# Kernel tuning notes

Measured on AMD Instinct MI355X. Metric: run time of the kernel, lower is better.

The kernel has to match this reference:

```python
import jax, jax.numpy as jnp
import numpy as np

B, N, E = 4, 2048, 1024
A, H = 64, 16          # attention_feature_dim, heads
D = A                   # per-head dim per source's rearrange quirk: d = attention_feature_dim
DK = A / H              # source scales by sqrt(attention_feature_dim / heads) = sqrt(4)
NEG_INF = jnp.float32(-jnp.inf)


def setup_inputs() -> dict:
    key = jax.random.key(0)
    ks = jax.random.split(key, 6)
    x = jax.random.normal(ks[0], (B, N, E), dtype=jnp.float32)
    mask = jax.random.randint(ks[1], (B, N), 0, 2, dtype=jnp.int32)
    # nn.Linear(E, A*H*3): weight [out,in] -> store transposed [in,out] for x @ W
    w_qkv = jax.random.normal(ks[2], (E, A * H * 3), dtype=jnp.float32) / np.sqrt(E)
    b_qkv = jax.random.normal(ks[3], (A * H * 3,), dtype=jnp.float32) * 0.02
    w_out = jax.random.normal(ks[4], (A * H, E), dtype=jnp.float32) / np.sqrt(A * H)
    b_out = jax.random.normal(ks[5], (E,), dtype=jnp.float32) * 0.02
    return {"x": x, "mask": mask, "w_qkv": w_qkv, "b_qkv": b_qkv,
            "w_out": w_out, "b_out": b_out}


def reference(x, mask, w_qkv, b_qkv, w_out, b_out):
    b, n, _ = x.shape
    qkv = x @ w_qkv + b_qkv                         # [b, n, 3*H*D]
    q, k, v = jnp.split(qkv, 3, axis=-1)            # each [b, n, H*D]
    def to_heads(t):
        return t.reshape(b, n, H, D).transpose(0, 2, 1, 3)  # [b, H, n, D]
    q, k, v = to_heads(q), to_heads(k), to_heads(v)
    scale = jnp.float32(1.0 / np.sqrt(DK))
    scores = jnp.einsum('bhqd,bhkd->bhqk', q, k) * scale    # [b, H, n, n]
    # mask: [b, n] -> [b, 1, 1, n]; masked positions (==0) get -inf
    scores = jnp.where(mask[:, None, None, :] == 0, NEG_INF, scores)
    attn = jax.nn.softmax(scores, axis=-1)
    out = jnp.einsum('bhqk,bhkd->bhqd', attn, v)            # [b, H, n, D]
    out = out.transpose(0, 2, 1, 3).reshape(b, n, H * D)    # [b, n, H*D]
    return out @ w_out + b_out                              # [b, n, E]
```

## Files before the change

### kernel.cpp

```cpp
#include <hip/hip_runtime.h>


typedef __bf16 bf16;
typedef __attribute__((ext_vector_type(8))) __bf16 bf16x8;
typedef __attribute__((ext_vector_type(4))) float f32x4;

#define MFMA16(a, b, c) __builtin_amdgcn_mfma_f32_16x16x32_bf16(a, b, c, 0, 0, 0)
#define GLOAD_LDS(src, dst) __builtin_amdgcn_global_load_lds( \
    (const __attribute__((address_space(1))) void*)(src),     \
    (__attribute__((address_space(3))) void*)(dst), 16, 0, 0)
#define BAR() __builtin_amdgcn_s_barrier()
#define VMCNT(n) asm volatile("s_waitcnt vmcnt(" #n ")" ::: "memory")

#define QSCALE 0.72134752f

__device__ __forceinline__ void transpose_tile(
    const float* __restrict__ in, bf16* __restrict__ out, int R, int C,
    int scale_rows, float scale, int bx, int by, int t, float (*s)[65])
{
    const int r0 = by * 64;
    const int c0 = bx * 64;
    const int tr  = t >> 4;
    const int tc4 = (t & 15) * 4;
#pragma unroll
    for (int p = 0; p < 4; ++p) {
        int r = tr + p * 16;
        float4 v = *(const float4*)(in + (size_t)(r0 + r) * C + c0 + tc4);
        s[r][tc4 + 0] = v.x; s[r][tc4 + 1] = v.y;
        s[r][tc4 + 2] = v.z; s[r][tc4 + 3] = v.w;
    }
    __syncthreads();
    const int cw  = t >> 3;
    const int rw8 = (t & 7) * 8;
#pragma unroll
    for (int p = 0; p < 2; ++p) {
        int c = cw + p * 32;
        float f = (c0 + c) < scale_rows ? scale : 1.0f;
        union { uint4 v; bf16 h[8]; } u;
#pragma unroll
        for (int j = 0; j < 8; ++j) u.h[j] = (bf16)(s[rw8 + j][c] * f);
        *(uint4*)(out + (size_t)(c0 + c) * R + r0 + rw8) = u.v;
    }
}

__global__ __launch_bounds__(256, 1) void prep_kernel(
    const float* __restrict__ x, bf16* __restrict__ xb,
    const float* __restrict__ w_qkv, bf16* __restrict__ wqkvT,
    const float* __restrict__ w_out, bf16* __restrict__ woutT)
{
    __shared__ float s[64][65];
    const int t = threadIdx.x;
    int blk = blockIdx.x;
    if (blk < 8192) {
        int i = blk * 256 + t;
        float4 v = *(const float4*)(x + (size_t)i * 4);
        union { ushort4 u; bf16 h[4]; } o;
        o.h[0] = (bf16)v.x; o.h[1] = (bf16)v.y;
        o.h[2] = (bf16)v.z; o.h[3] = (bf16)v.w;
        *(ushort4*)(xb + (size_t)i * 4) = o.u;
        return;
    }
    blk -= 8192;
    if (blk < 768) {
        transpose_tile(w_qkv, wqkvT, 1024, 3072, 1024, QSCALE,
                       blk % 48, blk / 48, t, s);
    } else {
        blk -= 768;
        transpose_tile(w_out, woutT, 1024, 1024, 0, 1.0f,
                       blk % 16, blk / 16, t, s);
    }
}

template <typename OutT>
__global__ __launch_bounds__(512, 2) void gemm128x256_kernel(
    const bf16* __restrict__ A, const bf16* __restrict__ Bt,
    const float* __restrict__ bias, OutT* __restrict__ C,
    int M, int N, int K, int qcols, float qscale, int nbx)
{
    __shared__ __align__(16) bf16 As[3 * 128 * 64];
    __shared__ __align__(16) bf16 Bs[3 * 256 * 64];

    const int t    = threadIdx.x;
    const int lane = t & 63;
    const int wave = t >> 6;
    const int wr   = wave >> 2;
    const int wc   = wave & 3;
    const int l15  = lane & 15;
    const int g    = lane >> 4;

    const int nwg  = gridDim.x;
    const int per  = nwg >> 3;
    const int mper = per / nbx;
    const int wg   = blockIdx.x;
    const int xcd  = wg & 7;
    const int idx  = wg >> 3;
    const int m0   = (xcd * mper + idx % mper) * 128;
    const int n0   = (idx / mper) * 256;

    const int ntile = K >> 6;

    int srow[2], sblk[2];
#pragma unroll
    for (int r = 0; r < 2; ++r) {
        int s = t * 16 + r * 8192;
        srow[r] = s >> 7;
        int blk = (s >> 4) & 7;
        sblk[r] = blk ^ (srow[r] & 7);
    }
    const int ldst0 = t * 8;

    const bf16* Abase = A  + (size_t)m0 * K;
    const bf16* Bbase = Bt + (size_t)n0 * K;

    const f32x4 z = {0.f, 0.f, 0.f, 0.f};
    f32x4 acc[4][4];
#pragma unroll
    for (int i = 0; i < 4; ++i)
#pragma unroll
        for (int j = 0; j < 4; ++j) acc[i][j] = z;

    auto stageA = [&](int tile, int slot) {
        if (tile >= ntile) return;
        bf16* dst = As + slot * 8192;
        const bf16* src = Abase + tile * 64;
#pragma unroll
        for (int r = 0; r < 2; ++r)
            GLOAD_LDS(src + (size_t)srow[r] * K + sblk[r] * 8,
                      dst + ldst0 + r * 4096);
    };
    auto stageBh = [&](int tile, int slot, int h) {
        if (tile >= ntile) return;
        bf16* dst = Bs + slot * 16384 + h * 8192;
        const bf16* src = Bbase + (size_t)(h * 128) * K + tile * 64;
#pragma unroll
        for (int r = 0; r < 2; ++r)
            GLOAD_LDS(src + (size_t)srow[r] * K + sblk[r] * 8,
                      dst + ldst0 + r * 4096);
    };

#define LOAD_AF(slot)                                                         \
    _Pragma("unroll")                                                         \
    for (int f = 0; f < 4; ++f) {                                             \
        int row = wr * 64 + f * 16 + l15;                                     \
        _Pragma("unroll")                                                     \
        for (int ks = 0; ks < 2; ++ks)                                        \
            af[f][ks] = *(const bf16x8*)(&As[(slot) * 8192 + row * 64 +       \
                            (((ks * 4 + g) ^ (row & 7)) * 8)]);               \
    }
#define LOAD_BF(slot, half, dstv)                                             \
    _Pragma("unroll")                                                         \
    for (int c2 = 0; c2 < 2; ++c2) {                                          \
        int row = wc * 64 + ((half) * 2 + c2) * 16 + l15;                     \
        _Pragma("unroll")                                                     \
        for (int ks = 0; ks < 2; ++ks)                                        \
            dstv[c2][ks] = *(const bf16x8*)(&Bs[(slot) * 16384 + row * 64 +   \
                            (((ks * 4 + g) ^ (row & 7)) * 8)]);               \
    }
#define MFMA_H(bv, half)                                                      \
    {                                                                         \
        __builtin_amdgcn_s_setprio(1);                                        \
        _Pragma("unroll")                                                     \
        for (int f = 0; f < 4; ++f)                                           \
            _Pragma("unroll")                                                 \
            for (int c2 = 0; c2 < 2; ++c2) {                                  \
                acc[f][(half) * 2 + c2] = MFMA16(                             \
                    af[f][0], bv[c2][0], acc[f][(half) * 2 + c2]);            \
                acc[f][(half) * 2 + c2] = MFMA16(                             \
                    af[f][1], bv[c2][1], acc[f][(half) * 2 + c2]);            \
            }                                                                 \
        __builtin_amdgcn_s_setprio(0);                                        \
    }

    stageA(0, 0); stageBh(0, 0, 0); stageBh(0, 0, 1);
    stageA(1, 1); stageBh(1, 1, 0); stageBh(1, 1, 1);
    VMCNT(6);
    BAR();

    int slot = 0;
    for (int T = 0; T < ntile; ++T) {
        int slot2 = slot + 2; if (slot2 >= 3) slot2 -= 3;
        bf16x8 af[4][2], blo[2][2], bhi[2][2];
        LOAD_AF(slot);
        LOAD_BF(slot, 0, blo);
        stageA(T + 2, slot2);
        stageBh(T + 2, slot2, 0);
        MFMA_H(blo, 0);
        BAR();
        LOAD_BF(slot, 1, bhi);
        stageBh(T + 2, slot2, 1);
        MFMA_H(bhi, 1);
        if (T + 1 < ntile) {
            if (T + 2 < ntile) { VMCNT(6); } else { VMCNT(0); }
        }
        BAR();
        slot = (slot == 2) ? 0 : slot + 1;
    }

#undef LOAD_AF
#undef LOAD_BF
#undef MFMA_H

#pragma unroll
    for (int f = 0; f < 4; ++f) {
        int row = m0 + wr * 64 + f * 16 + g * 4;
#pragma unroll
        for (int cf = 0; cf < 4; ++cf) {
            int col = n0 + wc * 64 + cf * 16 + l15;
            float bs = bias[col];
            if (col < qcols) bs *= qscale;
#pragma unroll
            for (int r = 0; r < 4; ++r) {
                float v = acc[f][cf][r] + bs;
                C[(size_t)(row + r) * N + col] = (OutT)v;
            }
        }
    }
}

__global__ __launch_bounds__(256, 1) void vtrans_kernel(
    const bf16* __restrict__ qkv, bf16* __restrict__ vtg)
{
    __shared__ float tile[64][65];
    const int t  = threadIdx.x;
    const int n0 = blockIdx.x * 64;
    const int bh = blockIdx.y;
    const int b  = bh >> 4, h = bh & 15;
    const bf16* src = qkv + (size_t)(b * 2048 + n0) * 3072 + 2048 + h * 64;
#pragma unroll
    for (int r = 0; r < 2; ++r) {
        int s = t + r * 256;
        int row = s >> 3, c8 = (s & 7) * 8;
        union { uint4 v; bf16 h8[8]; } u;
        u.v = *(const uint4*)(src + (size_t)row * 3072 + c8);
#pragma unroll
        for (int j = 0; j < 8; ++j) tile[row][c8 + j] = (float)u.h8[j];
    }
    __syncthreads();
    bf16* dst = vtg + (size_t)bh * (64 * 2048) + n0;
#pragma unroll
    for (int r = 0; r < 2; ++r) {
        int s = t + r * 256;
        int d = s >> 3, n8 = (s & 7) * 8;
        union { uint4 v; bf16 h8[8]; } o;
#pragma unroll
        for (int j = 0; j < 8; ++j) o.h8[j] = (bf16)tile[n8 + j][d];
        *(uint4*)(dst + (size_t)d * 2048 + n8) = o.v;
    }
}

__global__ __launch_bounds__(256, 3) void attn_kernel(
    const bf16* __restrict__ qkv, const bf16* __restrict__ vtg,
    const int* __restrict__ mask, bf16* __restrict__ O)
{
    __shared__ __align__(16) bf16 Ks[2][64 * 64];
    __shared__ __align__(16) bf16 Vt[2][64 * 64];
    __shared__ __align__(16) bf16 Ps[4][16 * 88];
    __shared__ __align__(16) float mneg[2048];

    const int t    = threadIdx.x;
    const int lane = t & 63;
    const int wave = t >> 6;
    const int l15  = lane & 15;
    const int g    = lane >> 4;

    const int bid = (blockIdx.x & 7) * 128 + (blockIdx.x >> 3);
    const int qt  = bid & 15;
    const int bh  = bid >> 4;
    const int h   = bh & 15;
    const int b   = bh >> 4;
    const int q0  = qt * 128 + wave * 16;

    const int* mrow = mask + b * 2048;
    for (int i = t; i < 2048; i += 256)
        mneg[i] = mrow[i] ? 0.0f : -1e30f;

    const size_t RS = 3072;
    const bf16* qp0 = qkv + (size_t)(b * 2048 + q0 + l15) * RS + h * 64 + g * 8;
    const bf16* qp1 = qp0 + (size_t)64 * RS;
    bf16x8 aQ[2][2];
    aQ[0][0] = *(const bf16x8*)(qp0);
    aQ[0][1] = *(const bf16x8*)(qp0 + 32);
    aQ[1][0] = *(const bf16x8*)(qp1);
    aQ[1][1] = *(const bf16x8*)(qp1 + 32);

    const bf16* kbase = qkv + (size_t)(b * 2048) * RS + 1024 + h * 64;
    const bf16* vbase = vtg + (size_t)bh * (64 * 2048);

    const int e0 = t * 8;
    int srow[2], scol[2];
#pragma unroll
    for (int r = 0; r < 2; ++r) {
        int e   = e0 + r * 2048;
        int row = e >> 6;
        int cb  = (e >> 3) & 7;
        srow[r] = row;
        scol[r] = ((cb ^ (row & 7)) * 8);
    }

    const int rb0 = ((g)     ^ (l15 & 7)) * 8;
    const int rb1 = ((4 + g) ^ (l15 & 7)) * 8;

    const f32x4 z = {0.f, 0.f, 0.f, 0.f};
    f32x4 o0[4] = {z, z, z, z}, o1[4] = {z, z, z, z};
    f32x4 lacc0 = z, lacc1 = z;

    bf16x8 ones;
#pragma unroll
    for (int j = 0; j < 8; ++j) ones[j] = (bf16)1.0f;

#pragma unroll
    for (int r = 0; r < 2; ++r) {
        GLOAD_LDS(kbase + (size_t)srow[r] * RS + scol[r],   &Ks[0][e0 + r * 2048]);
        GLOAD_LDS(vbase + (size_t)srow[r] * 2048 + scol[r], &Vt[0][e0 + r * 2048]);
    }
    asm volatile("s_waitcnt vmcnt(0)" ::: "memory");
    __syncthreads();

    for (int i = 0; i < 32; ++i) {
        const int kc  = i * 64;
        const int buf = i & 1;

        if (i + 1 < 32) {
#pragma unroll
            for (int r = 0; r < 2; ++r) {
                GLOAD_LDS(kbase + (size_t)(kc + 64 + srow[r]) * RS + scol[r],
                          &Ks[buf ^ 1][e0 + r * 2048]);
                GLOAD_LDS(vbase + (size_t)srow[r] * 2048 + kc + 64 + scol[r],
                          &Vt[buf ^ 1][e0 + r * 2048]);
            }
        }

        f32x4 mb4[4];
#pragma unroll
        for (int kt = 0; kt < 4; ++kt)
#pragma unroll
            for (int r = 0; r < 4; ++r)
                mb4[kt][r] = mneg[kc + kt * 16 + g * 4 + r];

        bf16x8 bk[4][2];
#pragma unroll
        for (int kt = 0; kt < 4; ++kt) {
            const bf16* kr = &Ks[buf][(kt * 16 + l15) * 64];
            bk[kt][0] = *(const bf16x8*)(kr + rb0);
            bk[kt][1] = *(const bf16x8*)(kr + rb1);
        }

        f32x4 S[4];
#pragma unroll
        for (int kt = 0; kt < 4; ++kt) {
            S[kt] = MFMA16(bk[kt][0], aQ[0][0], mb4[kt]);
            S[kt] = MFMA16(bk[kt][1], aQ[0][1], S[kt]);
        }
#pragma unroll
        for (int kt = 0; kt < 4; ++kt) {
            union { bf16 hh[4]; ushort4 u; } pk;
#pragma unroll
            for (int r = 0; r < 4; ++r)
                pk.hh[r] = (bf16)__builtin_amdgcn_exp2f(S[kt][r]);
            *(ushort4*)(&Ps[wave][l15 * 88 + kt * 16 + g * 4]) = pk.u;
        }
        asm volatile("s_waitcnt lgkmcnt(0)" ::: "memory");
        __builtin_amdgcn_sched_barrier(0);
        const bf16x8 aP00 = *(const bf16x8*)(&Ps[wave][l15 * 88 + g * 8]);
        const bf16x8 aP01 = *(const bf16x8*)(&Ps[wave][l15 * 88 + 32 + g * 8]);
        asm volatile("s_waitcnt lgkmcnt(0)" ::: "memory");
        __builtin_amdgcn_sched_barrier(0);

#pragma unroll
        for (int kt = 0; kt < 4; ++kt) {
            S[kt] = MFMA16(bk[kt][0], aQ[1][0], mb4[kt]);
            S[kt] = MFMA16(bk[kt][1], aQ[1][1], S[kt]);
        }

        bf16x8 bv[4][2];
#pragma unroll
        for (int dt = 0; dt < 4; ++dt) {
            const bf16* vr = &Vt[buf][(dt * 16 + l15) * 64];
            bv[dt][0] = *(const bf16x8*)(vr + rb0);
            bv[dt][1] = *(const bf16x8*)(vr + rb1);
        }

#pragma unroll
        for (int kt = 0; kt < 4; ++kt) {
            union { bf16 hh[4]; ushort4 u; } pk;
#pragma unroll
            for (int r = 0; r < 4; ++r)
                pk.hh[r] = (bf16)__builtin_amdgcn_exp2f(S[kt][r]);
            *(ushort4*)(&Ps[wave][l15 * 88 + kt * 16 + g * 4]) = pk.u;
        }

        lacc0 = MFMA16(aP00, ones, lacc0);
        lacc0 = MFMA16(aP01, ones, lacc0);
#pragma unroll
        for (int dt = 0; dt < 4; ++dt) {
            o0[dt] = MFMA16(aP00, bv[dt][0], o0[dt]);
            o0[dt] = MFMA16(aP01, bv[dt][1], o0[dt]);
        }
        asm volatile("s_waitcnt lgkmcnt(0)" ::: "memory");
        __builtin_amdgcn_sched_barrier(0);
        const bf16x8 aP10 = *(const bf16x8*)(&Ps[wave][l15 * 88 + g * 8]);
        const bf16x8 aP11 = *(const bf16x8*)(&Ps[wave][l15 * 88 + 32 + g * 8]);

        lacc1 = MFMA16(aP10, ones, lacc1);
        lacc1 = MFMA16(aP11, ones, lacc1);
#pragma unroll
        for (int dt = 0; dt < 4; ++dt) {
            o1[dt] = MFMA16(aP10, bv[dt][0], o1[dt]);
            o1[dt] = MFMA16(aP11, bv[dt][1], o1[dt]);
        }

        asm volatile("s_waitcnt vmcnt(0)" ::: "memory");
        __syncthreads();
    }

    float inv0[4], inv1[4];
#pragma unroll
    for (int r = 0; r < 4; ++r) {
        inv0[r] = 1.0f / fmaxf(lacc0[r], 1e-30f);
        inv1[r] = 1.0f / fmaxf(lacc1[r], 1e-30f);
    }
#pragma unroll
    for (int nt = 0; nt < 4; ++nt) {
#pragma unroll
        for (int r = 0; r < 4; ++r) {
            int d = nt * 16 + l15;
            int row0 = q0 + g * 4 + r;
            O[(size_t)(b * 2048 + row0) * 1024 + h * 64 + d] = (bf16)(o0[nt][r] * inv0[r]);
            O[(size_t)(b * 2048 + row0 + 64) * 1024 + h * 64 + d] = (bf16)(o1[nt][r] * inv1[r]);
        }
    }
}

extern "C" void kernel_launch(void* const* d_in, const int* in_sizes, int n_in,
                              void* d_out, int out_size, void* d_ws, size_t ws_size,
                              hipStream_t stream)
{
    const float* x     = (const float*)d_in[0];
    const int*   mask  = (const int*)d_in[1];
    const float* w_qkv = (const float*)d_in[2];
    const float* b_qkv = (const float*)d_in[3];
    const float* w_out = (const float*)d_in[4];
    const float* b_out = (const float*)d_in[5];
    float* out = (float*)d_out;

    char* ws = (char*)d_ws;
    bf16* qkvb  = (bf16*)(ws);
    bf16* Obuf  = (bf16*)(ws + 50331648);
    bf16* xb    = (bf16*)(ws + 67108864);
    bf16* wqkvT = (bf16*)(ws + 83886080);
    bf16* woutT = (bf16*)(ws + 90177536);
    bf16* vtg   = xb;

    prep_kernel<<<dim3(9216), 256, 0, stream>>>(x, xb, w_qkv, wqkvT, w_out, woutT);
    gemm128x256_kernel<bf16><<<dim3(768), 512, 0, stream>>>(
        xb, wqkvT, b_qkv, qkvb, 8192, 3072, 1024, 1024, QSCALE, 12);
    vtrans_kernel<<<dim3(32, 64), 256, 0, stream>>>(qkvb, vtg);
    attn_kernel<<<dim3(1024), 256, 0, stream>>>(qkvb, vtg, mask, Obuf);
    gemm128x256_kernel<float><<<dim3(256), 512, 0, stream>>>(
        Obuf, woutT, b_out, out, 8192, 1024, 1024, 0, 1.0f, 4);
}
```

Baseline: 277.0 us.

## Use 128x128 BK32 triple-buffered GEMM kernel for QKV projection

Adds a new GEMM kernel for the QKV projection with a 128x128 output tile, a K-step of 32, 256 threads and a three-slot LDS pipeline fed by direct global-to-LDS loads with an XOR swizzle. The grid doubles to 1536 workgroups, with a per-XCD tile mapping, to raise occupancy and smooth the tail. The trade-off is lower arithmetic intensity per tile and more barriers per unit of K work. The output projection keeps the old 128x256 kernel.

```diff
diff --git a/kernel.cpp b/kernel.cpp
--- a/kernel.cpp
+++ b/kernel.cpp
@@ -68,6 +68,121 @@
         blk -= 768;
         transpose_tile(w_out, woutT, 1024, 1024, 0, 1.0f,
                        blk % 16, blk / 16, t, s);
+    }
+}
+
+template <typename OutT>
+__global__ __launch_bounds__(256, 3) void gemm128bk32_kernel(
+    const bf16* __restrict__ A, const bf16* __restrict__ Bt,
+    const float* __restrict__ bias, OutT* __restrict__ C,
+    int M, int N, int K, int qcols, float qscale, int nbx)
+{
+    __shared__ __align__(16) bf16 As[3][128 * 32];
+    __shared__ __align__(16) bf16 Bs[3][128 * 32];
+
+    const int t    = threadIdx.x;
+    const int lane = t & 63;
+    const int wave = t >> 6;
+    const int wr   = wave >> 1;
+    const int wc   = wave & 1;
+    const int l15  = lane & 15;
+    const int g    = lane >> 4;
+
+    const int nwg  = gridDim.x;
+    const int per  = nwg >> 3;
+    const int mper = per / nbx;
+    const int wg   = blockIdx.x;
+    const int xcd  = wg & 7;
+    const int idx  = wg >> 3;
+    const int m0   = (xcd * mper + idx % mper) * 128;
+    const int n0   = (idx / mper) * 128;
+
+    const int ntile = K >> 5;
+
+    int srow[2], sblk[2];
+#pragma unroll
+    for (int r = 0; r < 2; ++r) {
+        int s = t * 16 + r * 4096;
+        srow[r] = s >> 6;
+        int blk = (s >> 4) & 3;
+        sblk[r] = blk ^ ((srow[r] >> 1) & 3);
+    }
+    const int ldst0 = t * 8;
+
+    const bf16* Abase = A  + (size_t)m0 * K;
+    const bf16* Bbase = Bt + (size_t)n0 * K;
+
+    const f32x4 z = {0.f, 0.f, 0.f, 0.f};
+    f32x4 acc[4][4];
+#pragma unroll
+    for (int i = 0; i < 4; ++i)
+#pragma unroll
+        for (int j = 0; j < 4; ++j) acc[i][j] = z;
+
+    auto stage = [&](int tile, int slot) {
+        if (tile >= ntile) return;
+        const bf16* asrc = Abase + tile * 32;
+        const bf16* bsrc = Bbase + tile * 32;
+#pragma unroll
+        for (int r = 0; r < 2; ++r) {
+            GLOAD_LDS(asrc + (size_t)srow[r] * K + sblk[r] * 8,
+                      &As[slot][ldst0 + r * 2048]);
+            GLOAD_LDS(bsrc + (size_t)srow[r] * K + sblk[r] * 8,
+                      &Bs[slot][ldst0 + r * 2048]);
+        }
+    };
+
+    stage(0, 0);
+    stage(1, 1);
+
+    int slot = 0;
+    for (int T = 0; T < ntile; ++T) {
+        int slot2 = slot + 2; if (slot2 >= 3) slot2 -= 3;
+        stage(T + 2, slot2);
+        if (T + 2 < ntile)      { VMCNT(8); }
+        else if (T + 1 < ntile) { VMCNT(4); }
+        else                    { VMCNT(0); }
+        BAR();
+
+        bf16x8 af[4], bf[4];
+#pragma unroll
+        for (int f = 0; f < 4; ++f) {
+            int row = wr * 64 + f * 16 + l15;
+            af[f] = *(const bf16x8*)(&As[slot][row * 32 +
+                        ((g ^ ((row >> 1) & 3)) * 8)]);
+        }
+#pragma unroll
+        for (int cf = 0; cf < 4; ++cf) {
+            int row = wc * 64 + cf * 16 + l15;
+            bf[cf] = *(const bf16x8*)(&Bs[slot][row * 32 +
+                        ((g ^ ((row >> 1) & 3)) * 8)]);
+        }
+
+        __builtin_amdgcn_s_setprio(1);
+#pragma unroll
+        for (int f = 0; f < 4; ++f)
+#pragma unroll
+            for (int cf = 0; cf < 4; ++cf)
+                acc[f][cf] = MFMA16(af[f], bf[cf], acc[f][cf]);
+        __builtin_amdgcn_s_setprio(0);
+        BAR();
+        slot = (slot == 2) ? 0 : slot + 1;
+    }
+
+#pragma unroll
+    for (int f = 0; f < 4; ++f) {
+        int row = m0 + wr * 64 + f * 16 + g * 4;
+#pragma unroll
+        for (int cf = 0; cf < 4; ++cf) {
+            int col = n0 + wc * 64 + cf * 16 + l15;
+            float bs = bias[col];
+            if (col < qcols) bs *= qscale;
+#pragma unroll
+            for (int r = 0; r < 4; ++r) {
+                float v = acc[f][cf][r] + bs;
+                C[(size_t)(row + r) * N + col] = (OutT)v;
+            }
+        }
     }
 }
 
@@ -452,8 +567,8 @@
     bf16* vtg   = xb;
 
     prep_kernel<<<dim3(9216), 256, 0, stream>>>(x, xb, w_qkv, wqkvT, w_out, woutT);
-    gemm128x256_kernel<bf16><<<dim3(768), 512, 0, stream>>>(
-        xb, wqkvT, b_qkv, qkvb, 8192, 3072, 1024, 1024, QSCALE, 12);
+    gemm128bk32_kernel<bf16><<<dim3(1536), 256, 0, stream>>>(
+        xb, wqkvT, b_qkv, qkvb, 8192, 3072, 1024, 1024, QSCALE, 24);
     vtrans_kernel<<<dim3(32, 64), 256, 0, stream>>>(qkvb, vtg);
     attn_kernel<<<dim3(1024), 256, 0, stream>>>(qkvb, vtg, mask, Obuf);
     gemm128x256_kernel<float><<<dim3(256), 512, 0, stream>>>(
```

Result: no change. 280.5 us (+1.2%).

## Fuse V transpose into QKV GEMM epilogue and drop vtrans kernel

Applied to the files above, without the earlier changes.

The QKV GEMM epilogue now writes V columns directly in transposed per-head layout (d-major, n contiguous) into a separate vtg buffer, and the qkv buffer keeps only Q and K with row stride 2048. The standalone vtrans kernel launch, and the V write and re-read it required, go away. In exchange, the V epilogue stores are 8-byte scattered writes with stride 2048 across d, which may coalesce worse than the row-major stores. The workspace layout is also reshuffled to fit the narrower qkv buffer and a dedicated vtg region.

```diff
diff --git a/kernel.cpp b/kernel.cpp
--- a/kernel.cpp
+++ b/kernel.cpp
@@ -75,7 +75,8 @@
 __global__ __launch_bounds__(512, 2) void gemm128x256_kernel(
     const bf16* __restrict__ A, const bf16* __restrict__ Bt,
     const float* __restrict__ bias, OutT* __restrict__ C,
-    int M, int N, int K, int qcols, float qscale, int nbx)
+    int M, int ldc, int K, int qcols, float qscale, int nbx,
+    bf16* __restrict__ vtg)
 {
     __shared__ __align__(16) bf16 As[3 * 128 * 64];
     __shared__ __align__(16) bf16 Bs[3 * 256 * 64];
@@ -200,51 +201,43 @@
 #undef LOAD_BF
 #undef MFMA_H
 
-#pragma unroll
-    for (int f = 0; f < 4; ++f) {
-        int row = m0 + wr * 64 + f * 16 + g * 4;
-#pragma unroll
-        for (int cf = 0; cf < 4; ++cf) {
-            int col = n0 + wc * 64 + cf * 16 + l15;
-            float bs = bias[col];
-            if (col < qcols) bs *= qscale;
-#pragma unroll
-            for (int r = 0; r < 4; ++r) {
-                float v = acc[f][cf][r] + bs;
-                C[(size_t)(row + r) * N + col] = (OutT)v;
+    if (vtg != nullptr && n0 >= 2048) {
+        const int b = m0 >> 11;
+#pragma unroll
+        for (int f = 0; f < 4; ++f) {
+            int row = m0 + wr * 64 + f * 16 + g * 4;
+            int n   = row & 2047;
+#pragma unroll
+            for (int cf = 0; cf < 4; ++cf) {
+                int col = n0 + wc * 64 + cf * 16 + l15;
+                int c2  = col - 2048;
+                int h   = c2 >> 6;
+                int d   = c2 & 63;
+                float bs = bias[col];
+                union { bf16 hh[4]; ushort4 u; } s;
+#pragma unroll
+                for (int r = 0; r < 4; ++r)
+                    s.hh[r] = (bf16)(acc[f][cf][r] + bs);
+                *(ushort4*)(vtg + (size_t)(b * 16 + h) * 131072 +
+                            (size_t)d * 2048 + n) = s.u;
             }
         }
-    }
-}
-
-__global__ __launch_bounds__(256, 1) void vtrans_kernel(
-    const bf16* __restrict__ qkv, bf16* __restrict__ vtg)
-{
-    __shared__ float tile[64][65];
-    const int t  = threadIdx.x;
-    const int n0 = blockIdx.x * 64;
-    const int bh = blockIdx.y;
-    const int b  = bh >> 4, h = bh & 15;
-    const bf16* src = qkv + (size_t)(b * 2048 + n0) * 3072 + 2048 + h * 64;
-#pragma unroll
-    for (int r = 0; r < 2; ++r) {
-        int s = t + r * 256;
-        int row = s >> 3, c8 = (s & 7) * 8;
-        union { uint4 v; bf16 h8[8]; } u;
-        u.v = *(const uint4*)(src + (size_t)row * 3072 + c8);
-#pragma unroll
-        for (int j = 0; j < 8; ++j) tile[row][c8 + j] = (float)u.h8[j];
-    }
-    __syncthreads();
-    bf16* dst = vtg + (size_t)bh * (64 * 2048) + n0;
-#pragma unroll
-    for (int r = 0; r < 2; ++r) {
-        int s = t + r * 256;
-        int d = s >> 3, n8 = (s & 7) * 8;
-        union { uint4 v; bf16 h8[8]; } o;
-#pragma unroll
-        for (int j = 0; j < 8; ++j) o.h8[j] = (bf16)tile[n8 + j][d];
-        *(uint4*)(dst + (size_t)d * 2048 + n8) = o.v;
+    } else {
+#pragma unroll
+        for (int f = 0; f < 4; ++f) {
+            int row = m0 + wr * 64 + f * 16 + g * 4;
+#pragma unroll
+            for (int cf = 0; cf < 4; ++cf) {
+                int col = n0 + wc * 64 + cf * 16 + l15;
+                float bs = bias[col];
+                if (col < qcols) bs *= qscale;
+#pragma unroll
+                for (int r = 0; r < 4; ++r) {
+                    float v = acc[f][cf][r] + bs;
+                    C[(size_t)(row + r) * ldc + col] = (OutT)v;
+                }
+            }
+        }
     }
 }
 
@@ -274,7 +267,7 @@
     for (int i = t; i < 2048; i += 256)
         mneg[i] = mrow[i] ? 0.0f : -1e30f;
 
-    const size_t RS = 3072;
+    const size_t RS = 2048;
     const bf16* qp0 = qkv + (size_t)(b * 2048 + q0 + l15) * RS + h * 64 + g * 8;
     const bf16* qp1 = qp0 + (size_t)64 * RS;
     bf16x8 aQ[2][2];
@@ -445,17 +438,16 @@
 
     char* ws = (char*)d_ws;
     bf16* qkvb  = (bf16*)(ws);
-    bf16* Obuf  = (bf16*)(ws + 50331648);
-    bf16* xb    = (bf16*)(ws + 67108864);
-    bf16* wqkvT = (bf16*)(ws + 83886080);
-    bf16* woutT = (bf16*)(ws + 90177536);
-    bf16* vtg   = xb;
+    bf16* Obuf  = (bf16*)(ws + 33554432);
+    bf16* xb    = (bf16*)(ws + 50331648);
+    bf16* wqkvT = (bf16*)(ws + 67108864);
+    bf16* woutT = (bf16*)(ws + 73400320);
+    bf16* vtg   = (bf16*)(ws + 75497472);
 
     prep_kernel<<<dim3(9216), 256, 0, stream>>>(x, xb, w_qkv, wqkvT, w_out, woutT);
     gemm128x256_kernel<bf16><<<dim3(768), 512, 0, stream>>>(
-        xb, wqkvT, b_qkv, qkvb, 8192, 3072, 1024, 1024, QSCALE, 12);
-    vtrans_kernel<<<dim3(32, 64), 256, 0, stream>>>(qkvb, vtg);
+        xb, wqkvT, b_qkv, qkvb, 8192, 2048, 1024, 1024, QSCALE, 12, vtg);
     attn_kernel<<<dim3(1024), 256, 0, stream>>>(qkvb, vtg, mask, Obuf);
     gemm128x256_kernel<float><<<dim3(256), 512, 0, stream>>>(
-        Obuf, woutT, b_out, out, 8192, 1024, 1024, 0, 1.0f, 4);
+        Obuf, woutT, b_out, out, 8192, 1024, 1024, 0, 1.0f, 4, nullptr);
 }
```

New measurement: 274.8 us. No clear change (-0.8%).
